# Kernel optimization log

Measured on AMD Instinct MI355X. Metric: run time of the kernel, lower is better.

The kernel has to match this reference:

```python
import jax, jax.numpy as jnp
import numpy as np

N = 50000
E = 800000
NFEAT, NHID, NCODE, NCLASS = 512, 256, 64, 40


def setup_inputs() -> dict:
    key = jax.random.key(0)
    ks = jax.random.split(key, 16)
    def glorot(k, shape):
        lim = 1.0 / np.sqrt(shape[0])
        return jax.random.uniform(k, shape, jnp.float32, -lim, lim)
    return {
        "x": jax.random.normal(ks[0], (N, NFEAT), jnp.float32),
        "edge_src": jax.random.randint(ks[1], (E,), 0, N, jnp.int32),
        "edge_dst": jax.random.randint(ks[2], (E,), 0, N, jnp.int32),
        "edge_weight": jax.random.uniform(ks[3], (E,), jnp.float32),
        "eps": jax.random.normal(ks[4], (N, NCODE), jnp.float32),
        # gc1: GraphConvolution(nfeat, nhid)
        "W1": glorot(ks[5], (NFEAT, NHID)),
        "b1": glorot(ks[6], (NHID,)),
        # fc11 / fc12: Linear(nhid, ncode)
        "W_mu": glorot(ks[7], (NHID, NCODE)),
        "b_mu": glorot(ks[8], (NCODE,)),
        "W_lv": glorot(ks[9], (NHID, NCODE)),
        "b_lv": glorot(ks[10], (NCODE,)),
        # fc2: Linear(ncode, nhid)
        "W_dec": glorot(ks[11], (NCODE, NHID)),
        "b_dec": glorot(ks[12], (NHID,)),
        # gc2: GraphConvolution(2*nhid, nclass)
        "W2": glorot(ks[13], (2 * NHID, NCLASS)),
        "b2": glorot(ks[14], (NCLASS,)),
    }


def spmm(edge_src, edge_dst, edge_weight, support):
    # spmm(adj, support): gather rows at src, scale by edge weight, scatter-add to dst
    msgs = support[edge_src] * edge_weight[:, None]  # [E, d]
    return jax.ops.segment_sum(msgs, edge_dst, num_segments=N)


def reference(x, edge_src, edge_dst, edge_weight, eps,
              W1, b1, W_mu, b_mu, W_lv, b_lv, W_dec, b_dec, W2, b2):
    # gc1: relu(spmm(adj, x @ W1) + b1)
    h1 = jax.nn.relu(spmm(edge_src, edge_dst, edge_weight, x @ W1) + b1)
    # dropout is identity in inference mode
    mu = h1 @ W_mu + b_mu
    log_var = h1 @ W_lv + b_lv
    # reparametrize: std = exp(log_var) (as in source, no 0.5 factor)
    z = mu + eps * jnp.exp(log_var)
    # decode
    x1 = jax.nn.relu(z @ W_dec + b_dec)
    x1 = jnp.concatenate([x1, h1], axis=1)  # [N, 2*nhid]
    # gc2
    logits = spmm(edge_src, edge_dst, edge_weight, x1 @ W2) + b2
    return jax.nn.log_softmax(logits, axis=1)
```

## Files before the change

### kernel.cpp

```cpp
#include <hip/hip_runtime.h>
#include <math.h>

#define N_NODES 50000
#define N_EDGES 800000
#define NFEAT 512
#define NHID 256
#define NCODE 64
#define NCLASS 40
#define NCLS_PAD 48
#define NB_SCAN 196

typedef __attribute__((ext_vector_type(8))) short short8;
typedef __attribute__((ext_vector_type(8))) unsigned short ushort8;
typedef __attribute__((ext_vector_type(4))) unsigned short ushort4v;
typedef __attribute__((ext_vector_type(4))) float floatx4;

__device__ inline unsigned short f2bf(float f) {
    unsigned u = __builtin_bit_cast(unsigned, f);
    u += 0x7fff + ((u >> 16) & 1);
    return (unsigned short)(u >> 16);
}
__device__ inline float bf2f(unsigned short h) {
    return __builtin_bit_cast(float, (unsigned)h << 16);
}
__device__ inline unsigned pkbf(float lo, float hi) {
    unsigned r;
    asm("v_cvt_pk_bf16_f32 %0, %1, %2" : "=v"(r) : "v"(lo), "v"(hi));
    return r;
}
__device__ inline void gload_lds16(const void* g, void* l) {
    __builtin_amdgcn_global_load_lds(
        (const __attribute__((address_space(1))) unsigned int*)g,
        (__attribute__((address_space(3))) unsigned int*)l, 16, 0, 0);
}

__global__ __launch_bounds__(256) void hist_kernel(const int* __restrict__ dst,
                                                   int* __restrict__ counts) {
    int t = blockIdx.x * 256 + threadIdx.x;
    if (t < N_EDGES) atomicAdd(&counts[dst[t]], 1);
}

__global__ __launch_bounds__(256) void scan_block_sums(const int* __restrict__ counts,
                                                       int* __restrict__ blockSums) {
    __shared__ int red[256];
    int t = threadIdx.x;
    int i = blockIdx.x * 256 + t;
    red[t] = (i < N_NODES) ? counts[i] : 0;
    __syncthreads();
#pragma unroll
    for (int off = 128; off > 0; off >>= 1) {
        if (t < off) red[t] += red[t + off];
        __syncthreads();
    }
    if (t == 0) blockSums[blockIdx.x] = red[0];
}

__global__ __launch_bounds__(256) void scan_block_offsets(const int* __restrict__ blockSums,
                                                          int* __restrict__ blockOffsets,
                                                          int* __restrict__ offsets) {
    __shared__ int s[256];
    int t = threadIdx.x;
    int v = (t < NB_SCAN) ? blockSums[t] : 0;
    s[t] = v;
    __syncthreads();
#pragma unroll
    for (int off = 1; off < 256; off <<= 1) {
        int x = (t >= off) ? s[t - off] : 0;
        __syncthreads();
        s[t] += x;
        __syncthreads();
    }
    if (t < NB_SCAN) blockOffsets[t] = s[t] - v;
    if (t == 255) offsets[N_NODES] = s[255];
}

__global__ __launch_bounds__(256) void scan_final(const int* __restrict__ counts,
                                                  const int* __restrict__ blockOffsets,
                                                  int* __restrict__ offsets) {
    __shared__ int s[256];
    int t = threadIdx.x;
    int i = blockIdx.x * 256 + t;
    int v = (i < N_NODES) ? counts[i] : 0;
    s[t] = v;
    __syncthreads();
#pragma unroll
    for (int off = 1; off < 256; off <<= 1) {
        int x = (t >= off) ? s[t - off] : 0;
        __syncthreads();
        s[t] += x;
        __syncthreads();
    }
    if (i < N_NODES) offsets[i] = blockOffsets[blockIdx.x] + s[t] - v;
}

__global__ __launch_bounds__(256) void scatter_kernel(const int* __restrict__ dst,
                                                      const int* __restrict__ src,
                                                      const float* __restrict__ w,
                                                      const int* __restrict__ offsets,
                                                      int* __restrict__ cursor,
                                                      int2* __restrict__ edges) {
    int t = blockIdx.x * 256 + threadIdx.x;
    if (t < N_EDGES) {
        int d = dst[t];
        int pos = offsets[d] + atomicAdd(&cursor[d], 1);
        edges[pos] = make_int2(src[t], __builtin_bit_cast(int, w[t]));
    }
}

__global__ __launch_bounds__(256) void wprep_kernel(const float* __restrict__ W1,
                                                    const float* __restrict__ W2,
                                                    const float* __restrict__ W_mu,
                                                    const float* __restrict__ W_lv,
                                                    const float* __restrict__ W_dec,
                                                    unsigned short* __restrict__ W1t,
                                                    unsigned short* __restrict__ W2bt,
                                                    unsigned short* __restrict__ W_mulvt,
                                                    unsigned short* __restrict__ W_dect) {
    int idx = blockIdx.x * 256 + threadIdx.x;
    if (idx < NFEAT * NHID) {
        int k = idx >> 8;
        int n = idx & 255;
        W1t[(size_t)n * NFEAT + k] = f2bf(W1[idx]);
    } else if (idx < NFEAT * NHID + NCLS_PAD * NFEAT) {
        int i2 = idx - NFEAT * NHID;
        int n = i2 >> 9;
        int k = i2 & 511;
        W2bt[i2] = (n < NCLASS) ? f2bf(W2[(size_t)k * NCLASS + n]) : (unsigned short)0;
    } else if (idx < NFEAT * NHID + NCLS_PAD * NFEAT + 128 * 256) {
        int i2 = idx - NFEAT * NHID - NCLS_PAD * NFEAT;
        int j = i2 >> 8;
        int k = i2 & 255;
        float v = (j < 64) ? W_mu[(size_t)k * NCODE + j] : W_lv[(size_t)k * NCODE + (j - 64)];
        W_mulvt[i2] = f2bf(v);
    } else if (idx < NFEAT * NHID + NCLS_PAD * NFEAT + 128 * 256 + 256 * 64) {
        int i2 = idx - NFEAT * NHID - NCLS_PAD * NFEAT - 128 * 256;
        int n = i2 >> 6;
        int k = i2 & 63;
        W_dect[i2] = f2bf(W_dec[(size_t)k * NHID + n]);
    }
}

__global__ __launch_bounds__(256) void gemm1_mfma(const float* __restrict__ A,
                                                  const unsigned short* __restrict__ Bt,
                                                  unsigned short* __restrict__ C) {
    __shared__ unsigned short As[128 * 64];
    __shared__ unsigned short Bs[128 * 64];
    int t = threadIdx.x;
    int wave = t >> 6, lane = t & 63;
    int quad = lane >> 4, m16 = lane & 15;
    int wr = wave >> 1, wc = wave & 1;
    int m0 = blockIdx.x * 128;
    int n0 = blockIdx.y * 128;

    int srow = t >> 3;
    int kcs = (t & 7) ^ (srow & 7);
    const float* Ap[4];
#pragma unroll
    for (int r = 0; r < 4; ++r) {
        int ga = m0 + r * 32 + srow;
        if (ga >= N_NODES) ga = N_NODES - 1;
        Ap[r] = A + (size_t)ga * NFEAT + kcs * 8;
    }
    const unsigned short* Bbase = Bt + (size_t)(n0 + srow) * NFEAT + kcs * 8;

    floatx4 acc[4][4];
#pragma unroll
    for (int m = 0; m < 4; ++m)
#pragma unroll
        for (int n = 0; n < 4; ++n) acc[m][n] = (floatx4){0.f, 0.f, 0.f, 0.f};

    float4 a0[4], a1[4];
#pragma unroll
    for (int r = 0; r < 4; ++r) {
        a0[r] = *(const float4*)(Ap[r]);
        a1[r] = *(const float4*)(Ap[r] + 4);
    }

#pragma unroll
    for (int k0 = 0; k0 < NFEAT; k0 += 64) {
        uint4 aw[4];
#pragma unroll
        for (int r = 0; r < 4; ++r) {
            aw[r].x = pkbf(a0[r].x, a0[r].y);
            aw[r].y = pkbf(a0[r].z, a0[r].w);
            aw[r].z = pkbf(a1[r].x, a1[r].y);
            aw[r].w = pkbf(a1[r].z, a1[r].w);
        }
        __syncthreads();
#pragma unroll
        for (int r = 0; r < 4; ++r)
            gload_lds16(Bbase + (size_t)r * 32 * NFEAT + k0, &Bs[(r * 256 + wave * 64) * 8]);
#pragma unroll
        for (int r = 0; r < 4; ++r) *(uint4*)&As[(r * 256 + t) * 8] = aw[r];
        __syncthreads();
        if (k0 + 64 < NFEAT) {
#pragma unroll
            for (int r = 0; r < 4; ++r) {
                a0[r] = *(const float4*)(Ap[r] + k0 + 64);
                a1[r] = *(const float4*)(Ap[r] + k0 + 68);
            }
        }
#pragma unroll
        for (int c = 0; c < 2; ++c) {
            int sw = ((c * 4 + quad) ^ (m16 & 7)) * 8;
            short8 af[4], bfr[4];
#pragma unroll
            for (int m = 0; m < 4; ++m)
                af[m] = *(const short8*)&As[(wr * 64 + m * 16 + m16) * 64 + sw];
#pragma unroll
            for (int n = 0; n < 4; ++n)
                bfr[n] = *(const short8*)&Bs[(wc * 64 + n * 16 + m16) * 64 + sw];
#pragma unroll
            for (int m = 0; m < 4; ++m)
#pragma unroll
                for (int n = 0; n < 4; ++n)
                    acc[m][n] =
                        __builtin_amdgcn_mfma_f32_16x16x32_bf16(af[m], bfr[n], acc[m][n], 0, 0, 0);
        }
    }
#pragma unroll
    for (int m = 0; m < 4; ++m) {
#pragma unroll
        for (int n = 0; n < 4; ++n) {
            int col = n0 + wc * 64 + n * 16 + m16;
#pragma unroll
            for (int r = 0; r < 4; ++r) {
                int row = m0 + wr * 64 + m * 16 + quad * 4 + r;
                if (row < N_NODES) C[(size_t)row * NHID + col] = f2bf(acc[m][n][r]);
            }
        }
    }
}

__global__ __launch_bounds__(256) void spmm1_kernel(const int* __restrict__ offsets,
                                                    const int2* __restrict__ edges,
                                                    const unsigned short* __restrict__ S1b,
                                                    const float* __restrict__ b1,
                                                    unsigned short* __restrict__ x1cat) {
    int n = blockIdx.x * 4 + (threadIdx.x >> 6);
    int lane = threadIdx.x & 63;
    int beg = offsets[n], end = offsets[n + 1];
    float ax = 0.f, ay = 0.f, az = 0.f, aw = 0.f;
    int i = beg;
    for (; i + 8 <= end; i += 8) {
        int2 e[8];
        ushort4v r[8];
#pragma unroll
        for (int u = 0; u < 8; u++) e[u] = edges[i + u];
#pragma unroll
        for (int u = 0; u < 8; u++)
            r[u] = *(const ushort4v*)&S1b[(size_t)e[u].x * NHID + lane * 4];
#pragma unroll
        for (int u = 0; u < 8; u++) {
            float ww = __builtin_bit_cast(float, e[u].y);
            ax += ww * bf2f(r[u][0]);
            ay += ww * bf2f(r[u][1]);
            az += ww * bf2f(r[u][2]);
            aw += ww * bf2f(r[u][3]);
        }
    }
    for (; i < end; i++) {
        int2 e = edges[i];
        float ww = __builtin_bit_cast(float, e.y);
        ushort4v r = *(const ushort4v*)&S1b[(size_t)e.x * NHID + lane * 4];
        ax += ww * bf2f(r[0]); ay += ww * bf2f(r[1]);
        az += ww * bf2f(r[2]); aw += ww * bf2f(r[3]);
    }
    float4 bb = *(const float4*)&b1[lane * 4];
    ushort4v hb;
    hb[0] = f2bf(fmaxf(ax + bb.x, 0.f));
    hb[1] = f2bf(fmaxf(ay + bb.y, 0.f));
    hb[2] = f2bf(fmaxf(az + bb.z, 0.f));
    hb[3] = f2bf(fmaxf(aw + bb.w, 0.f));
    *(ushort4v*)&x1cat[(size_t)n * (2 * NHID) + NHID + lane * 4] = hb;
}

__global__ __launch_bounds__(256) void mulv_mfma(const unsigned short* __restrict__ x1cat,
                                                 const unsigned short* __restrict__ W_mulvt,
                                                 const float* __restrict__ b_mu,
                                                 const float* __restrict__ b_lv,
                                                 unsigned short* __restrict__ mulv) {
    __shared__ unsigned short Bs[64][264];
    int t = threadIdx.x;
    int wave = t >> 6, lane = t & 63;
    int quad = lane >> 4, m16 = lane & 15;
    int m0 = blockIdx.x * 64;
    int ybase = blockIdx.y * 64;

#pragma unroll
    for (int r = 0; r < 8; ++r) {
        int c = r * 256 + t;
        int row = c >> 5, col = (c & 31) * 8;
        *(ushort8*)&Bs[row][col] = *(const ushort8*)&W_mulvt[(size_t)(ybase + row) * 256 + col];
    }
    int arow = m0 + wave * 16 + m16;
    if (arow >= N_NODES) arow = N_NODES - 1;
    const unsigned short* Abase = x1cat + (size_t)arow * 512 + 256 + quad * 8;

    floatx4 acc[4];
#pragma unroll
    for (int i = 0; i < 4; ++i) acc[i] = (floatx4){0.f, 0.f, 0.f, 0.f};
    __syncthreads();

#pragma unroll
    for (int k0 = 0; k0 < 256; k0 += 32) {
        short8 af = *(const short8*)(Abase + k0);
#pragma unroll
        for (int nt = 0; nt < 4; ++nt) {
            short8 bfr = *(const short8*)&Bs[nt * 16 + m16][k0 + quad * 8];
            acc[nt] = __builtin_amdgcn_mfma_f32_16x16x32_bf16(af, bfr, acc[nt], 0, 0, 0);
        }
    }
    const float* bias_v = blockIdx.y ? b_lv : b_mu;
#pragma unroll
    for (int nt = 0; nt < 4; ++nt) {
        int j = nt * 16 + m16;
        float bias = bias_v[j];
#pragma unroll
        for (int r = 0; r < 4; ++r) {
            int row = m0 + wave * 16 + quad * 4 + r;
            if (row < N_NODES) mulv[(size_t)row * 128 + ybase + j] = f2bf(acc[nt][r] + bias);
        }
    }
}

__global__ __launch_bounds__(256) void zdec_mfma(const unsigned short* __restrict__ mulv,
                                                 const float* __restrict__ eps,
                                                 const unsigned short* __restrict__ W_dect,
                                                 const float* __restrict__ b_dec,
                                                 unsigned short* __restrict__ x1cat) {
    __shared__ unsigned short Bs[256][72];
    int t = threadIdx.x;
    int wave = t >> 6, lane = t & 63;
    int quad = lane >> 4, m16 = lane & 15;
    int m0 = blockIdx.x * 64;

#pragma unroll
    for (int r = 0; r < 8; ++r) {
        int c = r * 256 + t;
        int row = c >> 3, col = (c & 7) * 8;
        *(ushort8*)&Bs[row][col] = *(const ushort8*)&W_dect[(size_t)row * 64 + col];
    }
    int grow = m0 + wave * 16 + m16;
    if (grow >= N_NODES) grow = N_NODES - 1;

    floatx4 acc[16];
#pragma unroll
    for (int i = 0; i < 16; ++i) acc[i] = (floatx4){0.f, 0.f, 0.f, 0.f};
    __syncthreads();

#pragma unroll
    for (int ks = 0; ks < 2; ++ks) {
        int c0 = ks * 32 + quad * 8;
        ushort8 mu8 = *(const ushort8*)&mulv[(size_t)grow * 128 + c0];
        ushort8 lv8 = *(const ushort8*)&mulv[(size_t)grow * 128 + 64 + c0];
        float4 e0 = *(const float4*)&eps[(size_t)grow * 64 + c0];
        float4 e1 = *(const float4*)&eps[(size_t)grow * 64 + c0 + 4];
        ushort8 zz;
        zz[0] = f2bf(bf2f(mu8[0]) + e0.x * expf(bf2f(lv8[0])));
        zz[1] = f2bf(bf2f(mu8[1]) + e0.y * expf(bf2f(lv8[1])));
        zz[2] = f2bf(bf2f(mu8[2]) + e0.z * expf(bf2f(lv8[2])));
        zz[3] = f2bf(bf2f(mu8[3]) + e0.w * expf(bf2f(lv8[3])));
        zz[4] = f2bf(bf2f(mu8[4]) + e1.x * expf(bf2f(lv8[4])));
        zz[5] = f2bf(bf2f(mu8[5]) + e1.y * expf(bf2f(lv8[5])));
        zz[6] = f2bf(bf2f(mu8[6]) + e1.z * expf(bf2f(lv8[6])));
        zz[7] = f2bf(bf2f(mu8[7]) + e1.w * expf(bf2f(lv8[7])));
        short8 af = *(short8*)&zz;
#pragma unroll
        for (int nt = 0; nt < 16; ++nt) {
            short8 bfr = *(const short8*)&Bs[nt * 16 + m16][ks * 32 + quad * 8];
            acc[nt] = __builtin_amdgcn_mfma_f32_16x16x32_bf16(af, bfr, acc[nt], 0, 0, 0);
        }
    }
#pragma unroll
    for (int nt = 0; nt < 16; ++nt) {
        int col = nt * 16 + m16;
        float bias = b_dec[col];
#pragma unroll
        for (int r = 0; r < 4; ++r) {
            int row = m0 + wave * 16 + quad * 4 + r;
            if (row < N_NODES)
                x1cat[(size_t)row * 512 + col] = f2bf(fmaxf(acc[nt][r] + bias, 0.f));
        }
    }
}

__global__ __launch_bounds__(256) void gemm2_mfma(const unsigned short* __restrict__ Xb,
                                                  const unsigned short* __restrict__ Bt,
                                                  unsigned short* __restrict__ S2b) {
    __shared__ unsigned short Bs[NCLS_PAD][520];
    int t = threadIdx.x;
    int wave = t >> 6, lane = t & 63;
    int quad = lane >> 4, m16 = lane & 15;
    int m0 = blockIdx.x * 64;

#pragma unroll
    for (int r = 0; r < 12; ++r) {
        int cidx = r * 256 + t;
        int row = cidx >> 6, col = (cidx & 63) * 8;
        *(ushort8*)&Bs[row][col] = *(const ushort8*)&Bt[(size_t)row * NFEAT + col];
    }

    int arow = m0 + wave * 16 + m16;
    if (arow >= N_NODES) arow = N_NODES - 1;
    const unsigned short* Abase = Xb + (size_t)arow * NFEAT + quad * 8;

    floatx4 acc[3];
#pragma unroll
    for (int i = 0; i < 3; i++) acc[i] = (floatx4){0.f, 0.f, 0.f, 0.f};
    __syncthreads();

#pragma unroll
    for (int k0 = 0; k0 < NFEAT; k0 += 32) {
        short8 af = *(const short8*)(Abase + k0);
#pragma unroll
        for (int nt = 0; nt < 3; nt++) {
            short8 bfr = *(const short8*)&Bs[nt * 16 + m16][k0 + quad * 8];
            acc[nt] = __builtin_amdgcn_mfma_f32_16x16x32_bf16(af, bfr, acc[nt], 0, 0, 0);
        }
    }
#pragma unroll
    for (int nt = 0; nt < 3; nt++) {
        int col = nt * 16 + m16;
        if (col < NCLASS) {
#pragma unroll
            for (int r = 0; r < 4; r++) {
                int row = m0 + wave * 16 + quad * 4 + r;
                if (row < N_NODES) S2b[(size_t)row * NCLASS + col] = f2bf(acc[nt][r]);
            }
        }
    }
}

__global__ __launch_bounds__(256) void spmm2_softmax_kernel(const int* __restrict__ offsets,
                                                            const int2* __restrict__ edges,
                                                            const unsigned short* __restrict__ S2b,
                                                            const float* __restrict__ b2,
                                                            float* __restrict__ out) {
    int wave = threadIdx.x >> 6;
    int lane = threadIdx.x & 63;
    int n = blockIdx.x * 4 + wave;
    int beg = offsets[n], end = offsets[n + 1];
    float acc = 0.f;
    int i = beg;
    for (; i + 4 <= end; i += 4) {
        int2 e0 = edges[i], e1 = edges[i + 1], e2 = edges[i + 2], e3 = edges[i + 3];
        float w0 = __builtin_bit_cast(float, e0.y);
        float w1 = __builtin_bit_cast(float, e1.y);
        float w2 = __builtin_bit_cast(float, e2.y);
        float w3 = __builtin_bit_cast(float, e3.y);
        if (lane < NCLASS) {
            float v0 = bf2f(S2b[(size_t)e0.x * NCLASS + lane]);
            float v1 = bf2f(S2b[(size_t)e1.x * NCLASS + lane]);
            float v2 = bf2f(S2b[(size_t)e2.x * NCLASS + lane]);
            float v3 = bf2f(S2b[(size_t)e3.x * NCLASS + lane]);
            acc += w0 * v0 + w1 * v1 + w2 * v2 + w3 * v3;
        }
    }
    for (; i < end; i++) {
        int2 e = edges[i];
        float ww = __builtin_bit_cast(float, e.y);
        if (lane < NCLASS) acc += ww * bf2f(S2b[(size_t)e.x * NCLASS + lane]);
    }
    float v = (lane < NCLASS) ? (acc + b2[lane]) : -INFINITY;
    float m = v;
#pragma unroll
    for (int off = 32; off > 0; off >>= 1) m = fmaxf(m, __shfl_xor(m, off));
    float ex = (lane < NCLASS) ? expf(v - m) : 0.f;
    float ssum = ex;
#pragma unroll
    for (int off = 32; off > 0; off >>= 1) ssum += __shfl_xor(ssum, off);
    if (lane < NCLASS) out[(size_t)n * NCLASS + lane] = v - m - logf(ssum);
}

extern "C" void kernel_launch(void* const* d_in, const int* in_sizes, int n_in,
                              void* d_out, int out_size, void* d_ws, size_t ws_size,
                              hipStream_t stream) {
    const float* x     = (const float*)d_in[0];
    const int*   esrc  = (const int*)d_in[1];
    const int*   edst  = (const int*)d_in[2];
    const float* ew    = (const float*)d_in[3];
    const float* eps   = (const float*)d_in[4];
    const float* W1    = (const float*)d_in[5];
    const float* b1    = (const float*)d_in[6];
    const float* W_mu  = (const float*)d_in[7];
    const float* b_mu  = (const float*)d_in[8];
    const float* W_lv  = (const float*)d_in[9];
    const float* b_lv  = (const float*)d_in[10];
    const float* W_dec = (const float*)d_in[11];
    const float* b_dec = (const float*)d_in[12];
    const float* W2    = (const float*)d_in[13];
    const float* b2    = (const float*)d_in[14];
    float* out = (float*)d_out;

    unsigned short* support1b = (unsigned short*)d_ws;
    unsigned short* x1cat = support1b + (size_t)N_NODES * NHID;
    unsigned short* S2b = x1cat + (size_t)N_NODES * 2 * NHID;
    unsigned short* W1t    = S2b + (size_t)N_NODES * NCLASS;
    unsigned short* W2bt   = W1t + (size_t)NHID * NFEAT;
    unsigned short* W_mulvt = W2bt + (size_t)NCLS_PAD * NFEAT;
    unsigned short* W_dect  = W_mulvt + 128 * 256;
    unsigned short* mulv    = W_dect + 256 * 64;
    int*   counts   = (int*)(((size_t)(mulv + (size_t)N_NODES * 128) + 3) & ~(size_t)3);
    int*   cursor   = counts + N_NODES;
    int*   offsets  = cursor + N_NODES;
    int*   blockSums    = offsets + N_NODES + 1;
    int*   blockOffsets = blockSums + NB_SCAN;
    int2*  edges    = (int2*)(blockOffsets + NB_SCAN);
    edges = (int2*)(((size_t)edges + 7) & ~(size_t)7);
    size_t need = (size_t)((char*)(edges + N_EDGES) - (char*)d_ws);
    if (ws_size < need) return;

    hipMemsetAsync(counts, 0, 2 * N_NODES * sizeof(int), stream);
    hist_kernel<<<(N_EDGES + 255) / 256, 256, 0, stream>>>(edst, counts);
    scan_block_sums<<<NB_SCAN, 256, 0, stream>>>(counts, blockSums);
    scan_block_offsets<<<1, 256, 0, stream>>>(blockSums, blockOffsets, offsets);
    scan_final<<<NB_SCAN, 256, 0, stream>>>(counts, blockOffsets, offsets);
    scatter_kernel<<<(N_EDGES + 255) / 256, 256, 0, stream>>>(edst, esrc, ew, offsets, cursor,
                                                              edges);

    wprep_kernel<<<800, 256, 0, stream>>>(W1, W2, W_mu, W_lv, W_dec, W1t, W2bt, W_mulvt, W_dect);
    dim3 g1((N_NODES + 127) / 128, 2);
    gemm1_mfma<<<g1, 256, 0, stream>>>(x, W1t, support1b);
    spmm1_kernel<<<N_NODES / 4, 256, 0, stream>>>(offsets, edges, support1b, b1, x1cat);
    dim3 gm((N_NODES + 63) / 64, 2);
    mulv_mfma<<<gm, 256, 0, stream>>>(x1cat, W_mulvt, b_mu, b_lv, mulv);
    zdec_mfma<<<(N_NODES + 63) / 64, 256, 0, stream>>>(mulv, eps, W_dect, b_dec, x1cat);
    gemm2_mfma<<<(N_NODES + 63) / 64, 256, 0, stream>>>(x1cat, W2bt, S2b);
    spmm2_softmax_kernel<<<N_NODES / 4, 256, 0, stream>>>(offsets, edges, S2b, b2, out);
}
```

Before: 437.5 us.

## Widen SpMM gathers to 16-byte loads with split-wave edge parallelism and padded S2 rows

Both SpMM kernels now have each lane load 8 bf16 values (16 bytes) per gather instead of 4 or 1. In spmm1 each half-wave processes alternate edges and the halves are combined with a cross-lane shuffle. In spmm2, S2 rows are padded to 64 columns with explicit zero-filled padding, so 8 lane groups can process 8 edges at once with full-width row loads. The log-softmax reductions are reworked to match. The aim is fewer, wider memory transactions and more gathers in flight per wave, at the cost of extra shuffles, a larger S2 buffer and some wasted padded bandwidth.

```diff
diff --git a/kernel.cpp b/kernel.cpp
--- a/kernel.cpp
+++ b/kernel.cpp
@@ -239,40 +239,54 @@
                                                     unsigned short* __restrict__ x1cat) {
     int n = blockIdx.x * 4 + (threadIdx.x >> 6);
     int lane = threadIdx.x & 63;
+    int h = lane >> 5;
+    int l32 = lane & 31;
     int beg = offsets[n], end = offsets[n + 1];
-    float ax = 0.f, ay = 0.f, az = 0.f, aw = 0.f;
+    float acc[8];
+#pragma unroll
+    for (int j = 0; j < 8; ++j) acc[j] = 0.f;
+
     int i = beg;
-    for (; i + 8 <= end; i += 8) {
+    for (; i + 16 <= end; i += 16) {
         int2 e[8];
-        ushort4v r[8];
-#pragma unroll
-        for (int u = 0; u < 8; u++) e[u] = edges[i + u];
-#pragma unroll
-        for (int u = 0; u < 8; u++)
-            r[u] = *(const ushort4v*)&S1b[(size_t)e[u].x * NHID + lane * 4];
-#pragma unroll
-        for (int u = 0; u < 8; u++) {
+        ushort8 r[8];
+#pragma unroll
+        for (int u = 0; u < 8; ++u) e[u] = edges[i + u * 2 + h];
+#pragma unroll
+        for (int u = 0; u < 8; ++u)
+            r[u] = *(const ushort8*)&S1b[(size_t)e[u].x * NHID + l32 * 8];
+#pragma unroll
+        for (int u = 0; u < 8; ++u) {
             float ww = __builtin_bit_cast(float, e[u].y);
-            ax += ww * bf2f(r[u][0]);
-            ay += ww * bf2f(r[u][1]);
-            az += ww * bf2f(r[u][2]);
-            aw += ww * bf2f(r[u][3]);
-        }
-    }
-    for (; i < end; i++) {
-        int2 e = edges[i];
-        float ww = __builtin_bit_cast(float, e.y);
-        ushort4v r = *(const ushort4v*)&S1b[(size_t)e.x * NHID + lane * 4];
-        ax += ww * bf2f(r[0]); ay += ww * bf2f(r[1]);
-        az += ww * bf2f(r[2]); aw += ww * bf2f(r[3]);
-    }
-    float4 bb = *(const float4*)&b1[lane * 4];
-    ushort4v hb;
-    hb[0] = f2bf(fmaxf(ax + bb.x, 0.f));
-    hb[1] = f2bf(fmaxf(ay + bb.y, 0.f));
-    hb[2] = f2bf(fmaxf(az + bb.z, 0.f));
-    hb[3] = f2bf(fmaxf(aw + bb.w, 0.f));
-    *(ushort4v*)&x1cat[(size_t)n * (2 * NHID) + NHID + lane * 4] = hb;
+#pragma unroll
+            for (int j = 0; j < 8; ++j) acc[j] += ww * bf2f(r[u][j]);
+        }
+    }
+    for (; i < end; i += 2) {
+        int idx = i + h;
+        int ic = (idx < end) ? idx : (end - 1);
+        int2 e = edges[ic];
+        float ww = (idx < end) ? __builtin_bit_cast(float, e.y) : 0.f;
+        ushort8 r = *(const ushort8*)&S1b[(size_t)e.x * NHID + l32 * 8];
+#pragma unroll
+        for (int j = 0; j < 8; ++j) acc[j] += ww * bf2f(r[j]);
+    }
+#pragma unroll
+    for (int j = 0; j < 8; ++j) acc[j] += __shfl_xor(acc[j], 32);
+    if (h == 0) {
+        float4 b0 = *(const float4*)&b1[l32 * 8];
+        float4 b4 = *(const float4*)&b1[l32 * 8 + 4];
+        ushort8 hb;
+        hb[0] = f2bf(fmaxf(acc[0] + b0.x, 0.f));
+        hb[1] = f2bf(fmaxf(acc[1] + b0.y, 0.f));
+        hb[2] = f2bf(fmaxf(acc[2] + b0.z, 0.f));
+        hb[3] = f2bf(fmaxf(acc[3] + b0.w, 0.f));
+        hb[4] = f2bf(fmaxf(acc[4] + b4.x, 0.f));
+        hb[5] = f2bf(fmaxf(acc[5] + b4.y, 0.f));
+        hb[6] = f2bf(fmaxf(acc[6] + b4.z, 0.f));
+        hb[7] = f2bf(fmaxf(acc[7] + b4.w, 0.f));
+        *(ushort8*)&x1cat[(size_t)n * (2 * NHID) + NHID + l32 * 8] = hb;
+    }
 }
 
 __global__ __launch_bounds__(256) void mulv_mfma(const unsigned short* __restrict__ x1cat,
@@ -422,13 +436,16 @@
 #pragma unroll
     for (int nt = 0; nt < 3; nt++) {
         int col = nt * 16 + m16;
-        if (col < NCLASS) {
-#pragma unroll
-            for (int r = 0; r < 4; r++) {
-                int row = m0 + wave * 16 + quad * 4 + r;
-                if (row < N_NODES) S2b[(size_t)row * NCLASS + col] = f2bf(acc[nt][r]);
-            }
-        }
+#pragma unroll
+        for (int r = 0; r < 4; r++) {
+            int row = m0 + wave * 16 + quad * 4 + r;
+            if (row < N_NODES) S2b[(size_t)row * 64 + col] = f2bf(acc[nt][r]);
+        }
+    }
+#pragma unroll
+    for (int r = 0; r < 4; r++) {
+        int row = m0 + wave * 16 + quad * 4 + r;
+        if (row < N_NODES) S2b[(size_t)row * 64 + 48 + m16] = 0;
     }
 }
 
@@ -439,38 +456,66 @@
                                                             float* __restrict__ out) {
     int wave = threadIdx.x >> 6;
     int lane = threadIdx.x & 63;
+    int g = lane >> 3, c = lane & 7;
     int n = blockIdx.x * 4 + wave;
     int beg = offsets[n], end = offsets[n + 1];
-    float acc = 0.f;
+    float acc[8];
+#pragma unroll
+    for (int j = 0; j < 8; ++j) acc[j] = 0.f;
+
     int i = beg;
-    for (; i + 4 <= end; i += 4) {
-        int2 e0 = edges[i], e1 = edges[i + 1], e2 = edges[i + 2], e3 = edges[i + 3];
+    for (; i + 16 <= end; i += 16) {
+        int2 e0 = edges[i + g];
+        int2 e1 = edges[i + 8 + g];
+        ushort8 r0 = *(const ushort8*)&S2b[(size_t)e0.x * 64 + c * 8];
+        ushort8 r1 = *(const ushort8*)&S2b[(size_t)e1.x * 64 + c * 8];
         float w0 = __builtin_bit_cast(float, e0.y);
         float w1 = __builtin_bit_cast(float, e1.y);
-        float w2 = __builtin_bit_cast(float, e2.y);
-        float w3 = __builtin_bit_cast(float, e3.y);
-        if (lane < NCLASS) {
-            float v0 = bf2f(S2b[(size_t)e0.x * NCLASS + lane]);
-            float v1 = bf2f(S2b[(size_t)e1.x * NCLASS + lane]);
-            float v2 = bf2f(S2b[(size_t)e2.x * NCLASS + lane]);
-            float v3 = bf2f(S2b[(size_t)e3.x * NCLASS + lane]);
-            acc += w0 * v0 + w1 * v1 + w2 * v2 + w3 * v3;
-        }
-    }
-    for (; i < end; i++) {
-        int2 e = edges[i];
-        float ww = __builtin_bit_cast(float, e.y);
-        if (lane < NCLASS) acc += ww * bf2f(S2b[(size_t)e.x * NCLASS + lane]);
-    }
-    float v = (lane < NCLASS) ? (acc + b2[lane]) : -INFINITY;
-    float m = v;
-#pragma unroll
-    for (int off = 32; off > 0; off >>= 1) m = fmaxf(m, __shfl_xor(m, off));
-    float ex = (lane < NCLASS) ? expf(v - m) : 0.f;
-    float ssum = ex;
-#pragma unroll
-    for (int off = 32; off > 0; off >>= 1) ssum += __shfl_xor(ssum, off);
-    if (lane < NCLASS) out[(size_t)n * NCLASS + lane] = v - m - logf(ssum);
+#pragma unroll
+        for (int j = 0; j < 8; ++j) acc[j] += w0 * bf2f(r0[j]) + w1 * bf2f(r1[j]);
+    }
+    for (; i < end; i += 8) {
+        int idx = i + g;
+        int ic = (idx < end) ? idx : (end - 1);
+        int2 e = edges[ic];
+        float ww = (idx < end) ? __builtin_bit_cast(float, e.y) : 0.f;
+        ushort8 r = *(const ushort8*)&S2b[(size_t)e.x * 64 + c * 8];
+#pragma unroll
+        for (int j = 0; j < 8; ++j) acc[j] += ww * bf2f(r[j]);
+    }
+#pragma unroll
+    for (int off = 8; off <= 32; off <<= 1) {
+#pragma unroll
+        for (int j = 0; j < 8; ++j) acc[j] += __shfl_xor(acc[j], off);
+    }
+    float v[8];
+#pragma unroll
+    for (int j = 0; j < 8; ++j) {
+        int col = c * 8 + j;
+        v[j] = (col < NCLASS) ? (acc[j] + b2[col]) : -INFINITY;
+    }
+    float m = v[0];
+#pragma unroll
+    for (int j = 1; j < 8; ++j) m = fmaxf(m, v[j]);
+#pragma unroll
+    for (int off = 1; off <= 4; off <<= 1) m = fmaxf(m, __shfl_xor(m, off));
+    float ssum = 0.f;
+    float ex[8];
+#pragma unroll
+    for (int j = 0; j < 8; ++j) {
+        ex[j] = (v[j] > -INFINITY) ? expf(v[j] - m) : 0.f;
+        ssum += ex[j];
+    }
+#pragma unroll
+    for (int off = 1; off <= 4; off <<= 1) ssum += __shfl_xor(ssum, off);
+    float lse = logf(ssum);
+    if (g == 0) {
+#pragma unroll
+        for (int j = 0; j < 8; ++j) {
+            int col = c * 8 + j;
+            if (col < NCLASS) out[(size_t)n * NCLASS + col] = v[j] - m - lse;
+        }
+    }
 }
 
 extern "C" void kernel_launch(void* const* d_in, const int* in_sizes, int n_in,
@@ -496,7 +541,7 @@
     unsigned short* support1b = (unsigned short*)d_ws;
     unsigned short* x1cat = support1b + (size_t)N_NODES * NHID;
     unsigned short* S2b = x1cat + (size_t)N_NODES * 2 * NHID;
-    unsigned short* W1t    = S2b + (size_t)N_NODES * NCLASS;
+    unsigned short* W1t    = S2b + (size_t)N_NODES * 64;
     unsigned short* W2bt   = W1t + (size_t)NHID * NFEAT;
     unsigned short* W_mulvt = W2bt + (size_t)NCLS_PAD * NFEAT;
     unsigned short* W_dect  = W_mulvt + 128 * 256;
```

Measured after the change: 456.9 us. 1.04x slower.
